# Kernel tuning notes

Hardware: AMD Instinct MI355X
Metric: run time of the kernel (lower is better)

## Reference

```python
import jax, jax.numpy as jnp
import numpy as np

B, S, D, H = 2, 2048, 1024, 16
HD = D // H  # head_dim = 64
THETA = 10000.0


def setup_inputs() -> dict:
    key = jax.random.key(0)
    ks = jax.random.split(key, 7)
    sd = 1.0 / np.sqrt(D)
    return {
        "hidden_states": jax.random.normal(ks[0], (B, S, D), jnp.float32),
        "attention_mask": jnp.ones((B, S), jnp.int32),
        "Wq": jax.random.normal(ks[1], (D, D), jnp.float32) * sd,
        "Wk": jax.random.normal(ks[2], (D, D), jnp.float32) * sd,
        "Wv": jax.random.normal(ks[3], (D, D), jnp.float32) * sd,
        "Wo": jax.random.normal(ks[4], (D, D), jnp.float32) * sd,
        "bo": jnp.zeros((D,), jnp.float32),
        "rel_bias": jax.random.normal(ks[5], (H, S, S), jnp.float32) * 0.02,
    }


def _rope_tables(seq_len):
    inv_freq = 1.0 / (THETA ** (jnp.arange(0, HD, 2, dtype=jnp.float32) / HD))  # [HD/2]
    freqs = jnp.arange(seq_len, dtype=jnp.float32)[:, None] * inv_freq[None, :]  # [S, HD/2]
    # add a heads axis for broadcasting against [B, S, H, HD/2]
    return jnp.cos(freqs)[:, None, :], jnp.sin(freqs)[:, None, :]


def _apply_rope(x, cos, sin):
    # x: [B, S, H, HD]; interleaved even/odd rotation
    x1, x2 = x[..., 0::2], x[..., 1::2]
    r1 = x1 * cos - x2 * sin
    r2 = x1 * sin + x2 * cos
    return jnp.stack([r1, r2], axis=-1).reshape(x.shape)


def reference(hidden_states, attention_mask, Wq, Wk, Wv, Wo, bo, rel_bias):
    b, s, d = hidden_states.shape
    q = (hidden_states @ Wq.T).reshape(b, s, H, HD)
    k = (hidden_states @ Wk.T).reshape(b, s, H, HD)
    v = (hidden_states @ Wv.T).reshape(b, s, H, HD)

    cos, sin = _rope_tables(s)
    q = _apply_rope(q, cos, sin)
    k = _apply_rope(k, cos, sin)

    scale = HD ** -0.5
    scores = jnp.einsum('bqhd,bkhd->bhqk', q, k) * scale + rel_bias[None]
    scores = jnp.where(attention_mask[:, None, None, :] == 0, -jnp.inf, scores)
    attn = jax.nn.softmax(scores, axis=-1)  # dropout is identity in eval
    out = jnp.einsum('bhqk,bkhd->bqhd', attn, v).reshape(b, s, d)
    return out @ Wo.T + bo
```

## Files before the change

kernel.cpp:

```cpp
#include <hip/hip_runtime.h>

typedef unsigned short u16;
typedef short bf16x8 __attribute__((ext_vector_type(8)));
typedef float f32x4 __attribute__((ext_vector_type(4)));
typedef unsigned short u16x4 __attribute__((ext_vector_type(4)));

typedef const __attribute__((address_space(1))) unsigned int* gas_ptr;
typedef __attribute__((address_space(3))) unsigned int* las_ptr;

__device__ __forceinline__ void gl_lds16(const void* g, void* l) {
  __builtin_amdgcn_global_load_lds((gas_ptr)g, (las_ptr)l, 16, 0, 0);
}

__device__ __forceinline__ u16 f2bf(float f) {
  union { float f; unsigned u; } v; v.f = f;
  unsigned r = v.u + 0x7FFFu + ((v.u >> 16) & 1u);
  return (u16)(r >> 16);
}

__device__ __forceinline__ float fexp2(float x) {
  float r; asm("v_exp_f32 %0, %1" : "=v"(r) : "v"(x)); return r;
}

__device__ __forceinline__ unsigned cvt_pk_bf16(float lo, float hi) {
  unsigned r;
  asm("v_cvt_pk_bf16_f32 %0, %1, %2" : "=v"(r) : "v"(lo), "v"(hi));
  return r;
}

__global__ void k_convert(const float* __restrict__ hs, const float* __restrict__ Wq,
                          const float* __restrict__ Wk, const float* __restrict__ Wv,
                          const float* __restrict__ Wo,
                          u16* __restrict__ Xb, u16* __restrict__ Wqkv, u16* __restrict__ Wob,
                          float* __restrict__ ctab, float* __restrict__ stab) {
  if (blockIdx.x >= 8192) {
    int t = (blockIdx.x - 8192) * 256 + threadIdx.x;
    int s = t >> 5, tt = t & 31;
    double f = exp(-((double)(2 * tt) / 64.0) * log(10000.0));
    double a = (double)s * f;
    ctab[t] = (float)cos(a);
    stab[t] = (float)sin(a);
    return;
  }
  int e = (blockIdx.x * 256 + threadIdx.x) * 4;
  const int R1 = 4096 * 1024, R2 = R1 + 3072 * 1024;
  float4 v; u16* dst;
  if (e < R1) {
    v = *(const float4*)&hs[e]; dst = Xb + e;
  } else if (e < R2) {
    int w = e - R1; int row = w >> 10, col = w & 1023;
    const float* src = row < 1024 ? &Wq[(size_t)row * 1024]
                     : (row < 2048 ? &Wk[(size_t)(row - 1024) * 1024]
                                   : &Wv[(size_t)(row - 2048) * 1024]);
    v = *(const float4*)&src[col]; dst = Wqkv + w;
  } else {
    int w = e - R2; v = *(const float4*)&Wo[w]; dst = Wob + w;
  }
  u16x4 o; o[0] = f2bf(v.x); o[1] = f2bf(v.y); o[2] = f2bf(v.z); o[3] = f2bf(v.w);
  *(u16x4*)dst = o;
}

__global__ __launch_bounds__(256, 3)
void k_gemm_qkv(const u16* __restrict__ A, const u16* __restrict__ B,
                const float* __restrict__ ctab, const float* __restrict__ stab,
                u16* __restrict__ Qb, u16* __restrict__ Kb, u16* __restrict__ Vtb,
                int K) {
  __shared__ u16 ldsA[128 * 64];
  __shared__ u16 ldsB[128 * 64];
  const int tid = threadIdx.x;
  const int g = blockIdx.y * 24 + blockIdx.x;
  const int xcd = g & 7, gi = g >> 3;
  const int bm = xcd * 4 + (gi & 3);
  const int bn = gi >> 2;
  const int lane = tid & 63, wave = tid >> 6;
  const int wm = wave >> 1, wn = wave & 1;
  const int l16 = lane & 15, quad = lane >> 4;

  const int srow = lane >> 3;
  const int scol = ((lane & 7) ^ srow) * 8;
  const u16* agb = A + (size_t)(bm * 128 + wave * 8 + srow) * K + scol;
  const u16* bgb = B + (size_t)(bn * 128 + wave * 8 + srow) * K + scol;

  const f32x4 vzero = {0.f, 0.f, 0.f, 0.f};
  f32x4 acc[4][4];
#pragma unroll
  for (int i = 0; i < 4; ++i)
#pragma unroll
    for (int j = 0; j < 4; ++j) acc[i][j] = vzero;

  const int xq = l16 & 7;
  const int NKT = K >> 6;
  for (int kt = 0; kt < NKT; ++kt) {
    __syncthreads();
#pragma unroll
    for (int p = 0; p < 4; ++p) {
      gl_lds16(agb + (size_t)p * 32 * K + kt * 64, &ldsA[(p * 4 + wave) * 512]);
      gl_lds16(bgb + (size_t)p * 32 * K + kt * 64, &ldsB[(p * 4 + wave) * 512]);
    }
    __syncthreads();
#pragma unroll
    for (int ks = 0; ks < 2; ++ks) {
      bf16x8 af[4], bfr[4];
#pragma unroll
      for (int mi = 0; mi < 4; ++mi)
        af[mi] = *(const bf16x8*)&ldsA[(wm * 64 + mi * 16 + l16) * 64 + ((ks * 4 + quad) ^ xq) * 8];
#pragma unroll
      for (int ni = 0; ni < 4; ++ni)
        bfr[ni] = *(const bf16x8*)&ldsB[(wn * 64 + ni * 16 + l16) * 64 + ((ks * 4 + quad) ^ xq) * 8];
#pragma unroll
      for (int mi = 0; mi < 4; ++mi)
#pragma unroll
        for (int ni = 0; ni < 4; ++ni)
          acc[mi][ni] = __builtin_amdgcn_mfma_f32_16x16x32_bf16(af[mi], bfr[ni], acc[mi][ni], 0, 0, 0);
    }
  }

  const int row0 = bm * 128 + wm * 64, col0 = bn * 128 + wn * 64;
  const int sect = bn >> 3;

  if (sect < 2) {
    u16* dst = sect == 0 ? Qb : Kb;
    const float mul = sect == 0 ? 0.18033688f : 1.0f;
#pragma unroll
    for (int mi = 0; mi < 4; ++mi)
#pragma unroll
      for (int ni = 0; ni < 4; ++ni) {
        int col = col0 + ni * 16 + l16;
        int cc = col & 1023;
        int h = cc >> 6, tt = (cc & 63) >> 1;
#pragma unroll
        for (int rr = 0; rr < 4; ++rr) {
          int row = row0 + mi * 16 + quad * 4 + rr;
          int s = row & 2047, bb = row >> 11;
          float x = acc[mi][ni][rr];
          float xo = __shfl_xor(x, 1);
          float x1 = (l16 & 1) ? xo : x;
          float x2 = (l16 & 1) ? x : xo;
          float cs = ctab[s * 32 + tt], sn = stab[s * 32 + tt];
          float r1 = (x1 * cs - x2 * sn) * mul;
          float r2 = (x1 * sn + x2 * cs) * mul;
          if (!(l16 & 1)) {
            union { u16 h2[2]; unsigned u; } o;
            o.h2[0] = f2bf(r1); o.h2[1] = f2bf(r2);
            *(unsigned*)&dst[((size_t)(bb * 16 + h) * 2048 + s) * 64 + (cc & 63)] = o.u;
          }
        }
      }
  } else {
#pragma unroll
    for (int mi = 0; mi < 4; ++mi)
#pragma unroll
      for (int ni = 0; ni < 4; ++ni) {
        int col = col0 + ni * 16 + l16;
        int cc = col & 1023;
        int h = cc >> 6, d = cc & 63;
        int row = row0 + mi * 16 + quad * 4;
        int s = row & 2047, bb = row >> 11;
        u16x4 o;
        o[0] = f2bf(acc[mi][ni][0]); o[1] = f2bf(acc[mi][ni][1]);
        o[2] = f2bf(acc[mi][ni][2]); o[3] = f2bf(acc[mi][ni][3]);
        *(u16x4*)&Vtb[((size_t)(bb * 16 + h) * 64 + d) * 2048 + s] = o;
      }
  }
}

__global__ __launch_bounds__(256, 4)
void k_attn(const u16* __restrict__ Qb, const u16* __restrict__ Kb, const u16* __restrict__ Vtb,
            const float* __restrict__ rel_bias, const int* __restrict__ mask,
            u16* __restrict__ Ob) {
  __shared__ u16 Ks[2][64 * 64];
  __shared__ u16 Vs[2][64 * 64];
  __shared__ u16 Ps[64 * 64];

  const int tid = threadIdx.x;
  const int gid = blockIdx.x;
  const int h = gid & 15, b = (gid >> 4) & 1, qt = gid >> 5;
  const int bh = b * 16 + h;
  const int lane = tid & 63, w = tid >> 6;
  const int l16 = lane & 15, quad = lane >> 4;
  const int xq = l16 & 7;

  bf16x8 qreg[2];
  {
    const u16* qg = Qb + ((size_t)bh * 2048 + qt * 64 + w * 16 + l16) * 64 + quad * 8;
    qreg[0] = *(const bf16x8*)&qg[0];
    qreg[1] = *(const bf16x8*)&qg[32];
  }

  const int srow = lane >> 3;
  const int scol = ((lane & 7) ^ srow) * 8;
  const u16* kgb = Kb + ((size_t)bh * 2048 + w * 8 + srow) * 64 + scol;
  const u16* vgb = Vtb + ((size_t)bh * 64 + w * 8 + srow) * 2048 + scol;

  const float* bp[4];
#pragma unroll
  for (int rr = 0; rr < 4; ++rr)
    bp[rr] = rel_bias + ((size_t)h * 2048 + qt * 64 + w * 16 + quad * 4 + rr) * 2048 + l16;
  const int* mbase = mask + b * 2048 + l16;

  const f32x4 vzero = {0.f, 0.f, 0.f, 0.f};
  f32x4 accO[4];
  float ls[4] = {0.f, 0.f, 0.f, 0.f};
#pragma unroll
  for (int ni = 0; ni < 4; ++ni) accO[ni] = vzero;

  float brc[4][4], brn[4][4];
#pragma unroll
  for (int ni = 0; ni < 4; ++ni) {
    int mk = mbase[ni * 16];
#pragma unroll
    for (int rr = 0; rr < 4; ++rr) {
      float bv = bp[rr][ni * 16];
      brc[ni][rr] = mk ? bv * 1.44269504f - 34.6246810f : -1e30f;
    }
  }
  gl_lds16(kgb,               &Ks[0][(0 * 4 + w) * 512]);
  gl_lds16(kgb + 2048,        &Ks[0][(1 * 4 + w) * 512]);
  gl_lds16(vgb,               &Vs[0][(0 * 4 + w) * 512]);
  gl_lds16(vgb + 32 * 2048,   &Vs[0][(1 * 4 + w) * 512]);

  for (int t = 0; t < 32; ++t) {
    const int cur = t & 1, nxt = cur ^ 1;
    const int kt0 = t * 64;
    __syncthreads();

    if (t + 1 < 32) {
      gl_lds16(kgb + (kt0 + 64) * 64,        &Ks[nxt][(0 * 4 + w) * 512]);
      gl_lds16(kgb + (kt0 + 64) * 64 + 2048, &Ks[nxt][(1 * 4 + w) * 512]);
      gl_lds16(vgb + kt0 + 64,               &Vs[nxt][(0 * 4 + w) * 512]);
      gl_lds16(vgb + kt0 + 64 + 32 * 2048,   &Vs[nxt][(1 * 4 + w) * 512]);
#pragma unroll
      for (int ni = 0; ni < 4; ++ni) {
        int mk = mbase[kt0 + 64 + ni * 16];
#pragma unroll
        for (int rr = 0; rr < 4; ++rr) {
          float bv = bp[rr][kt0 + 64 + ni * 16];
          brn[ni][rr] = mk ? bv * 1.44269504f - 34.6246810f : -1e30f;
        }
      }
    }

    f32x4 sa[4];
#pragma unroll
    for (int ni = 0; ni < 4; ++ni) sa[ni] = vzero;
#pragma unroll
    for (int ks = 0; ks < 2; ++ks) {
#pragma unroll
      for (int ni = 0; ni < 4; ++ni) {
        bf16x8 kf = *(const bf16x8*)&Ks[cur][(ni * 16 + l16) * 64 + ((ks * 4 + quad) ^ xq) * 8];
        sa[ni] = __builtin_amdgcn_mfma_f32_16x16x32_bf16(qreg[ks], kf, sa[ni], 0, 0, 0);
      }
    }

#pragma unroll
    for (int ni = 0; ni < 4; ++ni) {
#pragma unroll
      for (int rr = 0; rr < 4; ++rr) {
        float p = fexp2(sa[ni][rr] + brc[ni][rr]);
        ls[rr] += p;
        float po = __shfl_xor(p, 1);
        unsigned u = cvt_pk_bf16(p, po);
        if (!(l16 & 1)) {
          int prow = w * 16 + quad * 4 + rr;
          int chunk = (ni * 2 + (l16 >> 3)) ^ (prow & 7);
          *(unsigned*)&Ps[prow * 64 + chunk * 8 + (l16 & 7)] = u;
        }
      }
    }

#pragma unroll
    for (int ks = 0; ks < 2; ++ks) {
      bf16x8 pf = *(const bf16x8*)&Ps[(w * 16 + l16) * 64 + ((ks * 4 + quad) ^ xq) * 8];
#pragma unroll
      for (int ni = 0; ni < 4; ++ni) {
        bf16x8 vf = *(const bf16x8*)&Vs[cur][(ni * 16 + l16) * 64 + ((ks * 4 + quad) ^ xq) * 8];
        accO[ni] = __builtin_amdgcn_mfma_f32_16x16x32_bf16(pf, vf, accO[ni], 0, 0, 0);
      }
    }

#pragma unroll
    for (int ni = 0; ni < 4; ++ni)
#pragma unroll
      for (int rr = 0; rr < 4; ++rr) brc[ni][rr] = brn[ni][rr];
  }

#pragma unroll
  for (int rr = 0; rr < 4; ++rr) {
#pragma unroll
    for (int d = 1; d < 16; d <<= 1) ls[rr] += __shfl_xor(ls[rr], d, 16);
  }
#pragma unroll
  for (int rr = 0; rr < 4; ++rr) {
    float inv = 1.f / ls[rr];
    int row = qt * 64 + w * 16 + quad * 4 + rr;
#pragma unroll
    for (int ni = 0; ni < 4; ++ni)
      Ob[(((size_t)b * 2048 + row) * 16 + h) * 64 + ni * 16 + l16] = f2bf(accO[ni][rr] * inv);
  }
}

__global__ __launch_bounds__(256, 4)
void k_gemm_n64(const u16* __restrict__ A, const u16* __restrict__ B,
                const float* __restrict__ bias, float* __restrict__ C,
                int K, int ldc) {
  __shared__ u16 ldsA[128 * 64];
  __shared__ u16 ldsB[64 * 64];
  const int tid = threadIdx.x;
  const int g = blockIdx.y * 16 + blockIdx.x;
  const int xcd = g & 7, gi = g >> 3;
  const int bm = xcd * 4 + (gi & 3);
  const int bn = gi >> 2;
  const int lane = tid & 63, wave = tid >> 6;
  const int wm = wave >> 1, wn = wave & 1;
  const int l16 = lane & 15, quad = lane >> 4;

  const int srow = lane >> 3;
  const int scol = ((lane & 7) ^ srow) * 8;
  const u16* agb = A + (size_t)(bm * 128 + wave * 8 + srow) * K + scol;
  const u16* bgb = B + (size_t)(bn * 64 + wave * 8 + srow) * K + scol;

  const f32x4 vzero = {0.f, 0.f, 0.f, 0.f};
  f32x4 acc[4][2];
#pragma unroll
  for (int i = 0; i < 4; ++i)
#pragma unroll
    for (int j = 0; j < 2; ++j) acc[i][j] = vzero;

  const int xq = l16 & 7;
  const int NKT = K >> 6;
  for (int kt = 0; kt < NKT; ++kt) {
    __syncthreads();
#pragma unroll
    for (int p = 0; p < 4; ++p)
      gl_lds16(agb + (size_t)p * 32 * K + kt * 64, &ldsA[(p * 4 + wave) * 512]);
#pragma unroll
    for (int p = 0; p < 2; ++p)
      gl_lds16(bgb + (size_t)p * 32 * K + kt * 64, &ldsB[(p * 4 + wave) * 512]);
    __syncthreads();
#pragma unroll
    for (int ks = 0; ks < 2; ++ks) {
      bf16x8 af[4], bfr[2];
#pragma unroll
      for (int mi = 0; mi < 4; ++mi)
        af[mi] = *(const bf16x8*)&ldsA[(wm * 64 + mi * 16 + l16) * 64 + ((ks * 4 + quad) ^ xq) * 8];
#pragma unroll
      for (int ni = 0; ni < 2; ++ni)
        bfr[ni] = *(const bf16x8*)&ldsB[(wn * 32 + ni * 16 + l16) * 64 + ((ks * 4 + quad) ^ xq) * 8];
#pragma unroll
      for (int mi = 0; mi < 4; ++mi)
#pragma unroll
        for (int ni = 0; ni < 2; ++ni)
          acc[mi][ni] = __builtin_amdgcn_mfma_f32_16x16x32_bf16(af[mi], bfr[ni], acc[mi][ni], 0, 0, 0);
    }
  }

  const int row0 = bm * 128 + wm * 64, col0 = bn * 64 + wn * 32;
#pragma unroll
  for (int mi = 0; mi < 4; ++mi)
#pragma unroll
    for (int ni = 0; ni < 2; ++ni) {
      int col = col0 + ni * 16 + l16;
      float badd = bias ? bias[col] : 0.f;
#pragma unroll
      for (int rr = 0; rr < 4; ++rr) {
        int row = row0 + mi * 16 + quad * 4 + rr;
        C[(size_t)row * ldc + col] = acc[mi][ni][rr] + badd;
      }
    }
}

extern "C" void kernel_launch(void* const* d_in, const int* in_sizes, int n_in,
                              void* d_out, int out_size, void* d_ws, size_t ws_size,
                              hipStream_t stream) {
  (void)in_sizes; (void)n_in; (void)out_size; (void)ws_size;
  const float* hs  = (const float*)d_in[0];
  const int*   msk = (const int*)d_in[1];
  const float* Wq  = (const float*)d_in[2];
  const float* Wk  = (const float*)d_in[3];
  const float* Wv  = (const float*)d_in[4];
  const float* Wo  = (const float*)d_in[5];
  const float* bo  = (const float*)d_in[6];
  const float* rb  = (const float*)d_in[7];
  float* out = (float*)d_out;

  char* ws = (char*)d_ws;
  size_t off = 0;
  auto alloc = [&](size_t n) { char* p = ws + off; off += (n + 255) & ~(size_t)255; return p; };
  u16*   Xb   = (u16*)  alloc(4096UL * 1024 * 2);
  u16*   Wqkv = (u16*)  alloc(3072UL * 1024 * 2);
  u16*   Wob  = (u16*)  alloc(1024UL * 1024 * 2);
  u16*   Qb   = (u16*)  alloc(4096UL * 1024 * 2);
  u16*   Kb   = (u16*)  alloc(4096UL * 1024 * 2);
  u16*   Vtb  = (u16*)  alloc(4096UL * 1024 * 2);
  float* ctab = (float*)alloc(2048UL * 32 * 4);
  float* stab = (float*)alloc(2048UL * 32 * 4);
  u16*   Ob   = Xb;

  k_convert<<<8448, 256, 0, stream>>>(hs, Wq, Wk, Wv, Wo, Xb, Wqkv, Wob, ctab, stab);
  k_gemm_qkv<<<dim3(24, 32), 256, 0, stream>>>(Xb, Wqkv, ctab, stab, Qb, Kb, Vtb, 1024);
  k_attn<<<1024, 256, 0, stream>>>(Qb, Kb, Vtb, rb, msk, Ob);
  k_gemm_n64<<<dim3(16, 32), 256, 0, stream>>>(Ob, Wob, bo, out, 1024, 1024);
}
```

Before: 539.8 us.

## Double attention query tile to 128 rows with 8 waves sharing K/V tiles

The attention kernel now runs 512-thread blocks that each cover 128 query rows, so every K/V tile loaded into LDS is reused by twice as many waves. This halves global K/V traffic per query and means each thread issues one async load per tile instead of two. It also wraps both MFMA phases in s_setprio, writes P to LDS as single bf16 values instead of shuffling and packing pairs, and replaces the shuffle in the QKV RoPE epilogue with a DPP swap. The tighter launch bound (512, 6) may squeeze registers and cause spills. The larger block also means fewer blocks are resident per CU.

```diff
diff --git a/kernel.cpp b/kernel.cpp
--- a/kernel.cpp
+++ b/kernel.cpp
@@ -22,10 +22,9 @@
   float r; asm("v_exp_f32 %0, %1" : "=v"(r) : "v"(x)); return r;
 }
 
-__device__ __forceinline__ unsigned cvt_pk_bf16(float lo, float hi) {
-  unsigned r;
-  asm("v_cvt_pk_bf16_f32 %0, %1, %2" : "=v"(r) : "v"(lo), "v"(hi));
-  return r;
+__device__ __forceinline__ float swap1(float x) {
+  int i = __builtin_amdgcn_mov_dpp(__float_as_int(x), 0xB1, 0xF, 0xF, true);
+  return __int_as_float(i);
 }
 
 __global__ void k_convert(const float* __restrict__ hs, const float* __restrict__ Wq,
@@ -133,7 +132,7 @@
           int row = row0 + mi * 16 + quad * 4 + rr;
           int s = row & 2047, bb = row >> 11;
           float x = acc[mi][ni][rr];
-          float xo = __shfl_xor(x, 1);
+          float xo = swap1(x);
           float x1 = (l16 & 1) ? xo : x;
           float x2 = (l16 & 1) ? x : xo;
           float cs = ctab[s * 32 + tt], sn = stab[s * 32 + tt];
@@ -164,13 +163,13 @@
   }
 }
 
-__global__ __launch_bounds__(256, 4)
+__global__ __launch_bounds__(512, 6)
 void k_attn(const u16* __restrict__ Qb, const u16* __restrict__ Kb, const u16* __restrict__ Vtb,
             const float* __restrict__ rel_bias, const int* __restrict__ mask,
             u16* __restrict__ Ob) {
   __shared__ u16 Ks[2][64 * 64];
   __shared__ u16 Vs[2][64 * 64];
-  __shared__ u16 Ps[64 * 64];
+  __shared__ u16 Ps[128 * 64];
 
   const int tid = threadIdx.x;
   const int gid = blockIdx.x;
@@ -182,7 +181,7 @@
 
   bf16x8 qreg[2];
   {
-    const u16* qg = Qb + ((size_t)bh * 2048 + qt * 64 + w * 16 + l16) * 64 + quad * 8;
+    const u16* qg = Qb + ((size_t)bh * 2048 + qt * 128 + w * 16 + l16) * 64 + quad * 8;
     qreg[0] = *(const bf16x8*)&qg[0];
     qreg[1] = *(const bf16x8*)&qg[32];
   }
@@ -195,7 +194,7 @@
   const float* bp[4];
 #pragma unroll
   for (int rr = 0; rr < 4; ++rr)
-    bp[rr] = rel_bias + ((size_t)h * 2048 + qt * 64 + w * 16 + quad * 4 + rr) * 2048 + l16;
+    bp[rr] = rel_bias + ((size_t)h * 2048 + qt * 128 + w * 16 + quad * 4 + rr) * 2048 + l16;
   const int* mbase = mask + b * 2048 + l16;
 
   const f32x4 vzero = {0.f, 0.f, 0.f, 0.f};
@@ -214,10 +213,8 @@
       brc[ni][rr] = mk ? bv * 1.44269504f - 34.6246810f : -1e30f;
     }
   }
-  gl_lds16(kgb,               &Ks[0][(0 * 4 + w) * 512]);
-  gl_lds16(kgb + 2048,        &Ks[0][(1 * 4 + w) * 512]);
-  gl_lds16(vgb,               &Vs[0][(0 * 4 + w) * 512]);
-  gl_lds16(vgb + 32 * 2048,   &Vs[0][(1 * 4 + w) * 512]);
+  gl_lds16(kgb, &Ks[0][w * 512]);
+  gl_lds16(vgb, &Vs[0][w * 512]);
 
   for (int t = 0; t < 32; ++t) {
     const int cur = t & 1, nxt = cur ^ 1;
@@ -225,10 +222,8 @@
     __syncthreads();
 
     if (t + 1 < 32) {
-      gl_lds16(kgb + (kt0 + 64) * 64,        &Ks[nxt][(0 * 4 + w) * 512]);
-      gl_lds16(kgb + (kt0 + 64) * 64 + 2048, &Ks[nxt][(1 * 4 + w) * 512]);
-      gl_lds16(vgb + kt0 + 64,               &Vs[nxt][(0 * 4 + w) * 512]);
-      gl_lds16(vgb + kt0 + 64 + 32 * 2048,   &Vs[nxt][(1 * 4 + w) * 512]);
+      gl_lds16(kgb + (kt0 + 64) * 64, &Ks[nxt][w * 512]);
+      gl_lds16(vgb + kt0 + 64,        &Vs[nxt][w * 512]);
 #pragma unroll
       for (int ni = 0; ni < 4; ++ni) {
         int mk = mbase[kt0 + 64 + ni * 16];
@@ -243,6 +238,7 @@
     f32x4 sa[4];
 #pragma unroll
     for (int ni = 0; ni < 4; ++ni) sa[ni] = vzero;
+    __builtin_amdgcn_s_setprio(1);
 #pragma unroll
     for (int ks = 0; ks < 2; ++ks) {
 #pragma unroll
@@ -251,23 +247,20 @@
         sa[ni] = __builtin_amdgcn_mfma_f32_16x16x32_bf16(qreg[ks], kf, sa[ni], 0, 0, 0);
       }
     }
+    __builtin_amdgcn_s_setprio(0);
 
 #pragma unroll
     for (int ni = 0; ni < 4; ++ni) {
 #pragma unroll
       for (int rr = 0; rr < 4; ++rr) {
         float p = fexp2(sa[ni][rr] + brc[ni][rr]);
+        int prow = w * 16 + quad * 4 + rr;
+        Ps[prow * 64 + (((ni * 2 + (l16 >> 3)) ^ (prow & 7)) << 3) + (l16 & 7)] = f2bf(p);
         ls[rr] += p;
-        float po = __shfl_xor(p, 1);
-        unsigned u = cvt_pk_bf16(p, po);
-        if (!(l16 & 1)) {
-          int prow = w * 16 + quad * 4 + rr;
-          int chunk = (ni * 2 + (l16 >> 3)) ^ (prow & 7);
-          *(unsigned*)&Ps[prow * 64 + chunk * 8 + (l16 & 7)] = u;
-        }
-      }
-    }
-
+      }
+    }
+
+    __builtin_amdgcn_s_setprio(1);
 #pragma unroll
     for (int ks = 0; ks < 2; ++ks) {
       bf16x8 pf = *(const bf16x8*)&Ps[(w * 16 + l16) * 64 + ((ks * 4 + quad) ^ xq) * 8];
@@ -277,6 +270,7 @@
         accO[ni] = __builtin_amdgcn_mfma_f32_16x16x32_bf16(pf, vf, accO[ni], 0, 0, 0);
       }
     }
+    __builtin_amdgcn_s_setprio(0);
 
 #pragma unroll
     for (int ni = 0; ni < 4; ++ni)
@@ -292,7 +286,7 @@
 #pragma unroll
   for (int rr = 0; rr < 4; ++rr) {
     float inv = 1.f / ls[rr];
-    int row = qt * 64 + w * 16 + quad * 4 + rr;
+    int row = qt * 128 + w * 16 + quad * 4 + rr;
 #pragma unroll
     for (int ni = 0; ni < 4; ++ni)
       Ob[(((size_t)b * 2048 + row) * 16 + h) * 64 + ni * 16 + l16] = f2bf(accO[ni][rr] * inv);
@@ -398,6 +392,6 @@
 
   k_convert<<<8448, 256, 0, stream>>>(hs, Wq, Wk, Wv, Wo, Xb, Wqkv, Wob, ctab, stab);
   k_gemm_qkv<<<dim3(24, 32), 256, 0, stream>>>(Xb, Wqkv, ctab, stab, Qb, Kb, Vtb, 1024);
-  k_attn<<<1024, 256, 0, stream>>>(Qb, Kb, Vtb, rb, msk, Ob);
+  k_attn<<<512, 512, 0, stream>>>(Qb, Kb, Vtb, rb, msk, Ob);
   k_gemm_n64<<<dim3(16, 32), 256, 0, stream>>>(Ob, Wob, bo, out, 1024, 1024);
 }
```

After: 1.009 ms. 1.87x slower.
